# Kernel tuning notes

Measured on AMD Instinct MI355X. Metric: run time of the kernel, lower is better.

Reference implementation:

```python
import jax, jax.numpy as jnp
import numpy as np

KERNEL_SIZE = 5
SMOOTH_NR = 0.0
SMOOTH_DR = 1e-05


def _box_mean(x, k):
    # Depthwise 3D box (mean) filter via three separable 1-D convolutions.
    # x: [B, C, H, W, D]; zero padding 'SAME' matches F.conv3d(padding=(k-1)//2).
    C = x.shape[1]
    pad = (k - 1) // 2
    for axis in range(3):
        kshape = [1, 1, 1]
        kshape[axis] = k
        kern = jnp.full((C, 1) + tuple(kshape), 1.0 / k, dtype=x.dtype)
        padding = [(pad, pad) if i == axis else (0, 0) for i in range(3)]
        x = jax.lax.conv_general_dilated(
            x, kern, window_strides=(1, 1, 1), padding=padding,
            feature_group_count=C,
            dimension_numbers=('NCDHW', 'OIDHW', 'NCDHW'))
    return x


def setup_inputs() -> dict:
    key = jax.random.key(0)
    k1, k2 = jax.random.split(key)
    shape = (2, 1, 192, 192, 192)
    pred = jax.random.normal(k1, shape, dtype=jnp.float32)
    target = jax.random.normal(k2, shape, dtype=jnp.float32)
    return {"pred": pred, "target": target}


def reference(pred, target):
    k = KERNEL_SIZE
    # Local (windowed) means of the 5 intermediates: I, J, I^2, J^2, I*J.
    # Stack into a single 5C-channel tensor like ffo.create_intermediates,
    # then one grouped box filter (as in the original conv3d with groups=5C).
    C = pred.shape[1]
    interm = jnp.concatenate(
        [pred, target, pred * pred, target * target, pred * target], axis=1)
    m = _box_mean(interm, k)
    uI, uJ, I2, J2, IJ = jnp.split(m, 5, axis=1)
    cross = IJ - uI * uJ          # local covariance (mean form)
    var_i = I2 - uI * uI          # local variance of pred
    var_j = J2 - uJ * uJ          # local variance of target
    ncc = (cross * cross + SMOOTH_NR) / (var_i * var_j + SMOOTH_DR)
    # reduction='mean'; loss is negative squared local NCC
    return -jnp.mean(ncc)
```

## Files before the change

### kernel.cpp

```cpp
#include <hip/hip_runtime.h>

#define HH 192
#define WW 192
#define DD 192
#define BB 2
#define HCHUNK 40
#define NSLAB 5
#define SLICES (HCHUNK + 4)

#define PT_BUF   3200
#define PT_ROW   160
#define SQ_OFF   6400
#define OQ_OFF   9120
#define EQ_OFF   11840
#define SIJ_OFF  14560
#define OIJ_OFF  15200
#define EIJ_OFF  15840
#define LDS_BYTES 16480
#define QROW 272
#define IJROW 64

__global__ __launch_bounds__(256, 6)
void lncc_fused_kernel(const float* __restrict__ pred,
                       const float* __restrict__ targ,
                       double* __restrict__ acc_out) {
    __shared__ alignas(16) char lds[LDS_BYTES];
    __shared__ float wpart[4];

    const int tx = threadIdx.x, ty = threadIdx.y;
    const int tid = ty * 16 + tx;

    const int d0 = blockIdx.x * 16;
    const int w0 = blockIdx.y * 16;
    const int bz = blockIdx.z;
    const int b  = bz / NSLAB;
    const int h0 = (bz - b * NSLAB) * HCHUNK;
    const int base = b * (HH * WW * DD);

    const int syy = tid / 10;
    const int spx = tid - syy * 10;
    const int sw  = w0 - 2 + syy;
    const int sd  = d0 - 2 + 2 * spx;
    const bool s_ok = (tid < 200) & ((unsigned)sw < (unsigned)WW) & ((unsigned)sd < (unsigned)DD);
    const int spos = base + sw * DD + sd;
    char* const stW = lds + (syy * PT_ROW + spx * 16);

    const bool d_act = (tid < 80);
    const int dk = tid >> 3, dx = tid & 7;
    const char* const dR  = lds + (2 * dk * PT_ROW + dx * 16);
    char* const dWq  = lds + (SQ_OFF  + dk * QROW  + 2 * dx * 16);
    char* const dWij = lds + (SIJ_OFF + dk * IJROW + 2 * dx * 4);

    const int m = ty >> 1;
    const int osel = ty & 1;
    const char* const aQ1 = lds + (SQ_OFF + m * QROW + tx * 16 + (osel ? (OQ_OFF - SQ_OFF) : 0));
    const char* const aQ2 = lds + (SQ_OFF + (m + 1) * QROW + tx * 16);
    const char* const aQ3 = lds + (SQ_OFF + (m + 2) * QROW + tx * 16 + (osel ? 0 : (EQ_OFF - SQ_OFF)));
    const char* const aI1 = lds + (SIJ_OFF + m * IJROW + tx * 4 + (osel ? (OIJ_OFF - SIJ_OFF) : 0));
    const char* const aI2 = lds + (SIJ_OFF + (m + 1) * IJROW + tx * 4);
    const char* const aI3 = lds + (SIJ_OFF + (m + 2) * IJROW + tx * 4 + (osel ? 0 : (EIJ_OFF - SIJ_OFF)));

    float ring[5][5];
    float hs0 = 0.f, hs1 = 0.f, hs2 = 0.f, hs3 = 0.f, hs4 = 0.f;
#pragma unroll
    for (int q = 0; q < 5; ++q)
#pragma unroll
        for (int i = 0; i < 5; ++i) ring[q][i] = 0.f;
    float acc = 0.f;

#pragma unroll 2
    for (int it = 0; it < SLICES; ++it) {
        const int buf = it & 1;
        const int h = h0 - 2 + it;

        if (tid < 200) {
            float2 pv = make_float2(0.f, 0.f), tv = make_float2(0.f, 0.f);
            if (s_ok & ((unsigned)h < (unsigned)HH)) {
                const int idx = spos + h * (WW * DD);
                pv = *(const float2*)(pred + idx);
                tv = *(const float2*)(targ + idx);
            }
            *(float4*)(stW + buf * PT_BUF) = make_float4(pv.x, tv.x, pv.y, tv.y);
        }
        __syncthreads();

        if (d_act) {
            const char* R = dR + buf * PT_BUF;
            const float4 c0 = *(const float4*)(R);
            const float4 c1 = *(const float4*)(R + 16);
            const float4 c2 = *(const float4*)(R + 32);
            float ea0, ea1, ea2, ea3, ea4, eb0, eb1, eb2, eb3, eb4;
            {
                const float p0 = c0.x, q0 = c0.y, p1 = c0.z, q1 = c0.w;
                const float p2 = c1.x, q2 = c1.y, p3 = c1.z, q3 = c1.w;
                const float p4 = c2.x, q4 = c2.y, p5 = c2.z, q5 = c2.w;
                ea0 = p0 + p1 + p2 + p3 + p4;              eb0 = ea0 - p0 + p5;
                ea1 = q0 + q1 + q2 + q3 + q4;              eb1 = ea1 - q0 + q5;
                const float pp0 = p0 * p0, pp5 = p5 * p5;
                const float qq0 = q0 * q0, qq5 = q5 * q5;
                const float pq0 = p0 * q0, pq5 = p5 * q5;
                ea2 = pp0 + p1*p1 + p2*p2 + p3*p3 + p4*p4; eb2 = ea2 - pp0 + pp5;
                ea3 = qq0 + q1*q1 + q2*q2 + q3*q3 + q4*q4; eb3 = ea3 - qq0 + qq5;
                ea4 = pq0 + p1*q1 + p2*q2 + p3*q3 + p4*q4; eb4 = ea4 - pq0 + pq5;
            }
            *(float4*)(dWq + (EQ_OFF - SQ_OFF))      = make_float4(ea0, ea1, ea2, ea3);
            *(float4*)(dWq + (EQ_OFF - SQ_OFF) + 16) = make_float4(eb0, eb1, eb2, eb3);
            *(float2*)(dWij + (EIJ_OFF - SIJ_OFF))   = make_float2(ea4, eb4);
            const float4 c3 = *(const float4*)(R + PT_ROW);
            const float4 c4 = *(const float4*)(R + PT_ROW + 16);
            const float4 c5 = *(const float4*)(R + PT_ROW + 32);
            float oa0, oa1, oa2, oa3, oa4, ob0, ob1, ob2, ob3, ob4;
            {
                const float p0 = c3.x, q0 = c3.y, p1 = c3.z, q1 = c3.w;
                const float p2 = c4.x, q2 = c4.y, p3 = c4.z, q3 = c4.w;
                const float p4 = c5.x, q4 = c5.y, p5 = c5.z, q5 = c5.w;
                oa0 = p0 + p1 + p2 + p3 + p4;              ob0 = oa0 - p0 + p5;
                oa1 = q0 + q1 + q2 + q3 + q4;              ob1 = oa1 - q0 + q5;
                const float pp0 = p0 * p0, pp5 = p5 * p5;
                const float qq0 = q0 * q0, qq5 = q5 * q5;
                const float pq0 = p0 * q0, pq5 = p5 * q5;
                oa2 = pp0 + p1*p1 + p2*p2 + p3*p3 + p4*p4; ob2 = oa2 - pp0 + pp5;
                oa3 = qq0 + q1*q1 + q2*q2 + q3*q3 + q4*q4; ob3 = oa3 - qq0 + qq5;
                oa4 = pq0 + p1*q1 + p2*q2 + p3*q3 + p4*q4; ob4 = oa4 - pq0 + pq5;
            }
            *(float4*)(dWq + (OQ_OFF - SQ_OFF))      = make_float4(oa0, oa1, oa2, oa3);
            *(float4*)(dWq + (OQ_OFF - SQ_OFF) + 16) = make_float4(ob0, ob1, ob2, ob3);
            *(float2*)(dWij + (OIJ_OFF - SIJ_OFF))   = make_float2(oa4, ob4);
            *(float4*)(dWq)      = make_float4(ea0 + oa0, ea1 + oa1, ea2 + oa2, ea3 + oa3);
            *(float4*)(dWq + 16) = make_float4(eb0 + ob0, eb1 + ob1, eb2 + ob2, eb3 + ob3);
            *(float2*)(dWij)     = make_float2(ea4 + oa4, eb4 + ob4);
        }
        __syncthreads();

        const float4 Q1 = *(const float4*)aQ1;
        const float4 Q2 = *(const float4*)aQ2;
        const float4 Q3 = *(const float4*)aQ3;
        const float An0 = Q1.x + Q2.x + Q3.x;
        const float An1 = Q1.y + Q2.y + Q3.y;
        const float An2 = Q1.z + Q2.z + Q3.z;
        const float An3 = Q1.w + Q2.w + Q3.w;
        const float An4 = *(const float*)aI1 + *(const float*)aI2 + *(const float*)aI3;

        hs0 += An0 - ring[0][0];
        hs1 += An1 - ring[1][0];
        hs2 += An2 - ring[2][0];
        hs3 += An3 - ring[3][0];
        hs4 += An4 - ring[4][0];
#pragma unroll
        for (int q = 0; q < 5; ++q)
#pragma unroll
            for (int i = 0; i < 4; ++i) ring[q][i] = ring[q][i + 1];
        ring[0][4] = An0; ring[1][4] = An1; ring[2][4] = An2;
        ring[3][4] = An3; ring[4][4] = An4;

        if (it >= 4) {
            const int hout = h0 + it - 4;
            if (hout < HH) {
                const float inv = 1.0f / 125.0f;
                const float uI = hs0 * inv, uJ = hs1 * inv;
                const float I2 = hs2 * inv, J2 = hs3 * inv, IJ = hs4 * inv;
                const float cross = IJ - uI * uJ;
                const float vi = I2 - uI * uI;
                const float vj = J2 - uJ * uJ;
                acc += (cross * cross) * __builtin_amdgcn_rcpf(vi * vj + 1e-5f);
            }
        }
    }

#pragma unroll
    for (int off = 32; off > 0; off >>= 1) acc += __shfl_down(acc, off, 64);
    const int wid = tid >> 6, lane = tid & 63;
    if (lane == 0) wpart[wid] = acc;
    __syncthreads();
    if (tid == 0)
        atomicAdd(acc_out, (double)(wpart[0] + wpart[1] + wpart[2] + wpart[3]));
}

__global__ void lncc_finalize_kernel(const double* __restrict__ acc,
                                     float* __restrict__ out) {
    const double n = (double)BB * HH * WW * DD;
    out[0] = (float)(-acc[0] / n);
}

extern "C" void kernel_launch(void* const* d_in, const int* in_sizes, int n_in,
                              void* d_out, int out_size, void* d_ws, size_t ws_size,
                              hipStream_t stream) {
    const float* pred = (const float*)d_in[0];
    const float* targ = (const float*)d_in[1];
    float* out = (float*)d_out;
    double* acc = (double*)d_ws;

    hipMemsetAsync(d_ws, 0, sizeof(double), stream);

    dim3 grid(DD / 16, WW / 16, BB * NSLAB);
    dim3 block(16, 16, 1);
    lncc_fused_kernel<<<grid, block, 0, stream>>>(pred, targ, acc);
    lncc_finalize_kernel<<<1, 1, 0, stream>>>(acc, out);
}
```

Measured before the change: 205.2 us.

## Load slices directly to registers with prefetch and drop one barrier per slice

Producer threads now read their 6-wide d-span of pred/target straight from global memory into registers, prefetching the next slice while the current one is consumed. The raw-input LDS staging and the separate pairwise-sum pass are removed, which leaves one barrier per slice instead of two. Consumers read five W rows from a double-buffered LDS tile instead of three precombined pairs. The H chunk shrinks to give more blocks, and the launch bounds are raised to 8 waves per SIMD, so register pressure rises and each producer issues more global loads.

Measured after the change: 290.2 us. +41.4%, slower.

```diff
diff --git a/kernel.cpp b/kernel.cpp
--- a/kernel.cpp
+++ b/kernel.cpp
@@ -4,23 +4,19 @@
 #define WW 192
 #define DD 192
 #define BB 2
-#define HCHUNK 40
-#define NSLAB 5
+#define WWDD (WW * DD)
+#define HCHUNK 28
+#define NSLAB 7
 #define SLICES (HCHUNK + 4)
 
-#define PT_BUF   3200
-#define PT_ROW   160
-#define SQ_OFF   6400
-#define OQ_OFF   9120
-#define EQ_OFF   11840
-#define SIJ_OFF  14560
-#define OIJ_OFF  15200
-#define EIJ_OFF  15840
-#define LDS_BYTES 16480
 #define QROW 272
-#define IJROW 64
+#define QSIZE (20 * QROW)
+#define IJOFF QSIZE
+#define IJROW 72
+#define BUFSZ (QSIZE + 20 * IJROW)
+#define LDS_BYTES (2 * BUFSZ)
 
-__global__ __launch_bounds__(256, 6)
+__global__ __launch_bounds__(256, 8)
 void lncc_fused_kernel(const float* __restrict__ pred,
                        const float* __restrict__ targ,
                        double* __restrict__ acc_out) {
@@ -35,30 +31,23 @@
     const int bz = blockIdx.z;
     const int b  = bz / NSLAB;
     const int h0 = (bz - b * NSLAB) * HCHUNK;
-    const int base = b * (HH * WW * DD);
+    const int base = b * (HH * WWDD);
 
-    const int syy = tid / 10;
-    const int spx = tid - syy * 10;
-    const int sw  = w0 - 2 + syy;
-    const int sd  = d0 - 2 + 2 * spx;
-    const bool s_ok = (tid < 200) & ((unsigned)sw < (unsigned)WW) & ((unsigned)sd < (unsigned)DD);
-    const int spos = base + sw * DD + sd;
-    char* const stW = lds + (syy * PT_ROW + spx * 16);
+    const int k  = tid >> 3;
+    const int dx = tid & 7;
+    const int sw  = w0 - 2 + k;
+    const int sdb = d0 + 2 * dx - 2;
+    const bool prod   = (tid < 160);
+    const bool row_ok = prod && ((unsigned)sw < (unsigned)WW);
+    const bool ok0 = row_ok && (sdb >= 0);
+    const bool ok1 = row_ok;
+    const bool ok2 = row_ok && (sdb + 5 < DD);
+    const int  gofs = base + sw * DD + sdb;
+    char* const qW  = lds + (k * QROW + dx * 32);
+    char* const ijW = lds + (IJOFF + k * IJROW + dx * 8);
 
-    const bool d_act = (tid < 80);
-    const int dk = tid >> 3, dx = tid & 7;
-    const char* const dR  = lds + (2 * dk * PT_ROW + dx * 16);
-    char* const dWq  = lds + (SQ_OFF  + dk * QROW  + 2 * dx * 16);
-    char* const dWij = lds + (SIJ_OFF + dk * IJROW + 2 * dx * 4);
-
-    const int m = ty >> 1;
-    const int osel = ty & 1;
-    const char* const aQ1 = lds + (SQ_OFF + m * QROW + tx * 16 + (osel ? (OQ_OFF - SQ_OFF) : 0));
-    const char* const aQ2 = lds + (SQ_OFF + (m + 1) * QROW + tx * 16);
-    const char* const aQ3 = lds + (SQ_OFF + (m + 2) * QROW + tx * 16 + (osel ? 0 : (EQ_OFF - SQ_OFF)));
-    const char* const aI1 = lds + (SIJ_OFF + m * IJROW + tx * 4 + (osel ? (OIJ_OFF - SIJ_OFF) : 0));
-    const char* const aI2 = lds + (SIJ_OFF + (m + 1) * IJROW + tx * 4);
-    const char* const aI3 = lds + (SIJ_OFF + (m + 2) * IJROW + tx * 4 + (osel ? 0 : (EIJ_OFF - SIJ_OFF)));
+    const char* const qR  = lds + (ty * QROW + tx * 16);
+    const char* const ijR = lds + (IJOFF + ty * IJROW + tx * 4);
 
     float ring[5][5];
     float hs0 = 0.f, hs1 = 0.f, hs2 = 0.f, hs3 = 0.f, hs4 = 0.f;
@@ -68,78 +57,60 @@
         for (int i = 0; i < 5; ++i) ring[q][i] = 0.f;
     float acc = 0.f;
 
+    float2 P0, P1, P2, T0, T1, T2;
+    auto load_slice = [&](int h) {
+        P0 = P1 = P2 = T0 = T1 = T2 = make_float2(0.f, 0.f);
+        if ((unsigned)h < (unsigned)HH) {
+            const float* pp = pred + (gofs + h * WWDD);
+            const float* tt = targ + (gofs + h * WWDD);
+            if (ok0) { P0 = *(const float2*)pp;       T0 = *(const float2*)tt; }
+            if (ok1) { P1 = *(const float2*)(pp + 2); T1 = *(const float2*)(tt + 2); }
+            if (ok2) { P2 = *(const float2*)(pp + 4); T2 = *(const float2*)(tt + 4); }
+        }
+    };
+
+    load_slice(h0 - 2);
+
 #pragma unroll 2
     for (int it = 0; it < SLICES; ++it) {
-        const int buf = it & 1;
-        const int h = h0 - 2 + it;
+        const int buf = (it & 1) * BUFSZ;
 
-        if (tid < 200) {
-            float2 pv = make_float2(0.f, 0.f), tv = make_float2(0.f, 0.f);
-            if (s_ok & ((unsigned)h < (unsigned)HH)) {
-                const int idx = spos + h * (WW * DD);
-                pv = *(const float2*)(pred + idx);
-                tv = *(const float2*)(targ + idx);
-            }
-            *(float4*)(stW + buf * PT_BUF) = make_float4(pv.x, tv.x, pv.y, tv.y);
+        if (prod) {
+            const float p0 = P0.x, p1 = P0.y, p2 = P1.x, p3 = P1.y, p4 = P2.x, p5 = P2.y;
+            const float q0 = T0.x, q1 = T0.y, q2 = T1.x, q3 = T1.y, q4 = T2.x, q5 = T2.y;
+            const float ea0 = p0 + p1 + p2 + p3 + p4,             eb0 = ea0 - p0 + p5;
+            const float ea1 = q0 + q1 + q2 + q3 + q4,             eb1 = ea1 - q0 + q5;
+            const float pp0 = p0 * p0, pp5 = p5 * p5;
+            const float qq0 = q0 * q0, qq5 = q5 * q5;
+            const float pq0 = p0 * q0, pq5 = p5 * q5;
+            const float ea2 = pp0 + p1*p1 + p2*p2 + p3*p3 + p4*p4, eb2 = ea2 - pp0 + pp5;
+            const float ea3 = qq0 + q1*q1 + q2*q2 + q3*q3 + q4*q4, eb3 = ea3 - qq0 + qq5;
+            const float ea4 = pq0 + p1*q1 + p2*q2 + p3*q3 + p4*q4, eb4 = ea4 - pq0 + pq5;
+            *(float4*)(qW + buf)      = make_float4(ea0, ea1, ea2, ea3);
+            *(float4*)(qW + buf + 16) = make_float4(eb0, eb1, eb2, eb3);
+            *(float2*)(ijW + buf)     = make_float2(ea4, eb4);
         }
+
+        if (it + 1 < SLICES) load_slice(h0 - 1 + it);
+
         __syncthreads();
 
-        if (d_act) {
-            const char* R = dR + buf * PT_BUF;
-            const float4 c0 = *(const float4*)(R);
-            const float4 c1 = *(const float4*)(R + 16);
-            const float4 c2 = *(const float4*)(R + 32);
-            float ea0, ea1, ea2, ea3, ea4, eb0, eb1, eb2, eb3, eb4;
-            {
-                const float p0 = c0.x, q0 = c0.y, p1 = c0.z, q1 = c0.w;
-                const float p2 = c1.x, q2 = c1.y, p3 = c1.z, q3 = c1.w;
-                const float p4 = c2.x, q4 = c2.y, p5 = c2.z, q5 = c2.w;
-                ea0 = p0 + p1 + p2 + p3 + p4;              eb0 = ea0 - p0 + p5;
-                ea1 = q0 + q1 + q2 + q3 + q4;              eb1 = ea1 - q0 + q5;
-                const float pp0 = p0 * p0, pp5 = p5 * p5;
-                const float qq0 = q0 * q0, qq5 = q5 * q5;
-                const float pq0 = p0 * q0, pq5 = p5 * q5;
-                ea2 = pp0 + p1*p1 + p2*p2 + p3*p3 + p4*p4; eb2 = ea2 - pp0 + pp5;
-                ea3 = qq0 + q1*q1 + q2*q2 + q3*q3 + q4*q4; eb3 = ea3 - qq0 + qq5;
-                ea4 = pq0 + p1*q1 + p2*q2 + p3*q3 + p4*q4; eb4 = ea4 - pq0 + pq5;
-            }
-            *(float4*)(dWq + (EQ_OFF - SQ_OFF))      = make_float4(ea0, ea1, ea2, ea3);
-            *(float4*)(dWq + (EQ_OFF - SQ_OFF) + 16) = make_float4(eb0, eb1, eb2, eb3);
-            *(float2*)(dWij + (EIJ_OFF - SIJ_OFF))   = make_float2(ea4, eb4);
-            const float4 c3 = *(const float4*)(R + PT_ROW);
-            const float4 c4 = *(const float4*)(R + PT_ROW + 16);
-            const float4 c5 = *(const float4*)(R + PT_ROW + 32);
-            float oa0, oa1, oa2, oa3, oa4, ob0, ob1, ob2, ob3, ob4;
-            {
-                const float p0 = c3.x, q0 = c3.y, p1 = c3.z, q1 = c3.w;
-                const float p2 = c4.x, q2 = c4.y, p3 = c4.z, q3 = c4.w;
-                const float p4 = c5.x, q4 = c5.y, p5 = c5.z, q5 = c5.w;
-                oa0 = p0 + p1 + p2 + p3 + p4;              ob0 = oa0 - p0 + p5;
-                oa1 = q0 + q1 + q2 + q3 + q4;              ob1 = oa1 - q0 + q5;
-                const float pp0 = p0 * p0, pp5 = p5 * p5;
-                const float qq0 = q0 * q0, qq5 = q5 * q5;
-                const float pq0 = p0 * q0, pq5 = p5 * q5;
-                oa2 = pp0 + p1*p1 + p2*p2 + p3*p3 + p4*p4; ob2 = oa2 - pp0 + pp5;
-                oa3 = qq0 + q1*q1 + q2*q2 + q3*q3 + q4*q4; ob3 = oa3 - qq0 + qq5;
-                oa4 = pq0 + p1*q1 + p2*q2 + p3*q3 + p4*q4; ob4 = oa4 - pq0 + pq5;
-            }
-            *(float4*)(dWq + (OQ_OFF - SQ_OFF))      = make_float4(oa0, oa1, oa2, oa3);
-            *(float4*)(dWq + (OQ_OFF - SQ_OFF) + 16) = make_float4(ob0, ob1, ob2, ob3);
-            *(float2*)(dWij + (OIJ_OFF - SIJ_OFF))   = make_float2(oa4, ob4);
-            *(float4*)(dWq)      = make_float4(ea0 + oa0, ea1 + oa1, ea2 + oa2, ea3 + oa3);
-            *(float4*)(dWq + 16) = make_float4(eb0 + ob0, eb1 + ob1, eb2 + ob2, eb3 + ob3);
-            *(float2*)(dWij)     = make_float2(ea4 + oa4, eb4 + ob4);
-        }
-        __syncthreads();
-
-        const float4 Q1 = *(const float4*)aQ1;
-        const float4 Q2 = *(const float4*)aQ2;
-        const float4 Q3 = *(const float4*)aQ3;
-        const float An0 = Q1.x + Q2.x + Q3.x;
-        const float An1 = Q1.y + Q2.y + Q3.y;
-        const float An2 = Q1.z + Q2.z + Q3.z;
-        const float An3 = Q1.w + Q2.w + Q3.w;
-        const float An4 = *(const float*)aI1 + *(const float*)aI2 + *(const float*)aI3;
+        const char* rq = qR + buf;
+        const float4 Q0 = *(const float4*)(rq);
+        const float4 Q1 = *(const float4*)(rq + QROW);
+        const float4 Q2 = *(const float4*)(rq + 2 * QROW);
+        const float4 Q3 = *(const float4*)(rq + 3 * QROW);
+        const float4 Q4 = *(const float4*)(rq + 4 * QROW);
+        const char* ri = ijR + buf;
+        const float An0 = Q0.x + Q1.x + Q2.x + Q3.x + Q4.x;
+        const float An1 = Q0.y + Q1.y + Q2.y + Q3.y + Q4.y;
+        const float An2 = Q0.z + Q1.z + Q2.z + Q3.z + Q4.z;
+        const float An3 = Q0.w + Q1.w + Q2.w + Q3.w + Q4.w;
+        const float An4 = *(const float*)(ri)
+                        + *(const float*)(ri + IJROW)
+                        + *(const float*)(ri + 2 * IJROW)
+                        + *(const float*)(ri + 3 * IJROW)
+                        + *(const float*)(ri + 4 * IJROW);
 
         hs0 += An0 - ring[0][0];
         hs1 += An1 - ring[1][0];
```
